# Optimization experiments

Hardware: AMD Instinct MI355X
Metric: run time of the kernel (lower is better)

## Reference

```python
import jax, jax.numpy as jnp
import numpy as np

RCUT = 6.0       # rcut
RMIN = 0.5       # rcut_smth
NF, NLOC, NALL, NNEI = 4, 4096, 4096, 128
AXIS = 8         # axis_neuron
EPS = 1e-12


def setup_inputs() -> dict:
    key = jax.random.key(0)
    ks = jax.random.split(key, 8)
    coord = jax.random.normal(ks[0], (NF, NALL, 3), dtype=jnp.float32) * 2.0
    nlist = jax.random.randint(ks[1], (NF, NLOC, NNEI), 0, NALL, dtype=jnp.int32)
    davg = jnp.zeros((NNEI, 4), dtype=jnp.float32)
    dstd = jnp.ones((NNEI, 4), dtype=jnp.float32)
    w1 = jax.random.normal(ks[2], (1, 24), dtype=jnp.float32) * 0.5
    b1 = jax.random.normal(ks[3], (24,), dtype=jnp.float32) * 0.1
    w2 = jax.random.normal(ks[4], (24, 48), dtype=jnp.float32) * 0.2
    b2 = jax.random.normal(ks[5], (48,), dtype=jnp.float32) * 0.1
    w3 = jax.random.normal(ks[6], (48, 96), dtype=jnp.float32) * 0.15
    b3 = jax.random.normal(ks[7], (96,), dtype=jnp.float32) * 0.1
    return {"coord": coord, "davg": davg, "dstd": dstd,
            "w1": w1, "b1": b1, "w2": w2, "b2": b2, "w3": w3, "b3": b3,
            "nlist": nlist}


def _embed(x, w1, b1, w2, b2, w3, b3):
    # DeepMD embedding net: tanh layers, resnet skip via duplication when dim doubles
    h1 = jnp.tanh(x @ w1 + b1)                                   # [..., 24]
    h2 = jnp.tanh(h1 @ w2 + b2) + jnp.concatenate([h1, h1], -1)  # [..., 48]
    h3 = jnp.tanh(h2 @ w3 + b3) + jnp.concatenate([h2, h2], -1)  # [..., 96]
    return h3


def reference(coord, davg, dstd, w1, b1, w2, b2, w3, b3, nlist):
    # gather neighbor coordinates: [nf, nloc, nnei, 3]
    coord_nei = jax.vmap(lambda c, nl: c[nl])(coord, nlist)
    rij = coord_nei - coord[:, :NLOC, None, :]
    r = jnp.sqrt(jnp.sum(rij * rij, axis=-1) + EPS)              # [nf, nloc, nnei]
    # smooth switching function
    uu = (r - RMIN) / (RCUT - RMIN)
    sw_mid = uu * uu * uu * (-6.0 * uu * uu + 15.0 * uu - 10.0) + 1.0
    sw = jnp.where(r < RMIN, 1.0, jnp.where(r < RCUT, sw_mid, 0.0))
    s = sw / r                                                    # [nf, nloc, nnei]
    # environment matrix R: [s, s*x/r, s*y/r, s*z/r] -> [nf, nloc, nnei, 4]
    env = jnp.concatenate([s[..., None], s[..., None] * rij / r[..., None]], axis=-1)
    env = (env - davg) / dstd
    # per-pair embedding of the radial channel
    G = _embed(env[..., :1], w1, b1, w2, b2, w3, b3)              # [nf, nloc, nnei, 96]
    # axis contraction: T = R^T G / nnei -> [nf, nloc, 4, 96]
    T = jnp.einsum('flnd,flnm->fldm', env, G) / NNEI
    # descriptor D = T^T T[:, :axis] -> [nf, nloc, 96, 8]
    D = jnp.einsum('fldm,fldk->flmk', T, T[..., :AXIS])
    return D.reshape(NF, NLOC, 96 * AXIS)
```

## Files before the change

kernel.cpp:

```cpp
#include <hip/hip_runtime.h>
#include <hip/hip_bf16.h>
#include <cstdint>

#define NF_   4
#define NLOC_ 4096
#define NALL_ 4096
#define NNEI_ 128
#define RCUT_ 6.0f
#define RMIN_ 0.5f

typedef __attribute__((ext_vector_type(8))) short    bhalf8;
typedef __attribute__((ext_vector_type(4))) float    f32x4;
typedef __attribute__((ext_vector_type(4))) unsigned u32x4;

__device__ __forceinline__ float fast_tanh(float x) {
    float e = __expf(2.0f * x);
    return 1.0f - 2.0f * __builtin_amdgcn_rcpf(e + 1.0f);
}
__device__ __forceinline__ unsigned short bfb(float v) {
    return __builtin_bit_cast(unsigned short, __float2bfloat16(v));
}
__device__ __forceinline__ float bff(unsigned short b) {
    return __builtin_bit_cast(float, (unsigned)b << 16);
}
__device__ __forceinline__ unsigned pk(float a, float b) {
    return (unsigned)bfb(a) | ((unsigned)bfb(b) << 16);
}
__device__ __forceinline__ float bf16_lo(unsigned u) {
    return __builtin_bit_cast(float, u << 16);
}
__device__ __forceinline__ float bf16_hi(unsigned u) {
    return __builtin_bit_cast(float, u & 0xffff0000u);
}

__global__ void prepack_weights(const float* __restrict__ w2,
                                const float* __restrict__ w3,
                                unsigned* __restrict__ ws) {
    const int idx = threadIdx.x + blockIdx.x * 256;
    if (idx < 768) {
        const int u   = idx & 3;
        const int l   = (idx >> 2) & 63;
        const int mt  = idx >> 8;
        const int m16 = l & 15, kg = l >> 4;
        const int k0  = 8 * kg + 2 * u;
        const unsigned short s0 = (k0 < 24)     ? bfb(w2[k0 * 48 + 16 * mt + m16])       : (unsigned short)0;
        const unsigned short s1 = (k0 + 1 < 24) ? bfb(w2[(k0 + 1) * 48 + 16 * mt + m16]) : (unsigned short)0;
        ws[idx] = (unsigned)s0 | ((unsigned)s1 << 16);
    } else if (idx < 3840) {
        const int j   = idx - 768;
        const int u   = j & 3;
        const int l   = (j >> 2) & 63;
        const int nt  = (j >> 8) & 1;
        const int ks  = (j >> 9) & 1;
        const int sb  = j >> 10;
        const int m16 = l & 15, kg = l >> 4;
        const int k0  = 32 * ks + 8 * kg + 2 * u;
        const int col = 32 * sb + 16 * nt + m16;
        const unsigned short s0 = (k0 < 48)     ? bfb(w3[k0 * 96 + col])       : (unsigned short)0;
        const unsigned short s1 = (k0 + 1 < 48) ? bfb(w3[(k0 + 1) * 96 + col]) : (unsigned short)0;
        ws[idx] = (unsigned)s0 | ((unsigned)s1 << 16);
    }
}

__global__ __launch_bounds__(128, 4)
void descrpt_sea_kernel(
    const float* __restrict__ coord,
    const float* __restrict__ davg,
    const float* __restrict__ dstd,
    const float* __restrict__ w1, const float* __restrict__ b1,
    const float* __restrict__ w2, const float* __restrict__ b2,
    const float* __restrict__ w3, const float* __restrict__ b3,
    const int*   __restrict__ nlist,
    const unsigned* __restrict__ wsp,
    float* __restrict__ out)
{
    __shared__ __align__(16) unsigned smem[6016];
    float*    envs = (float*)smem;
    unsigned* h1L  = smem + 512;
    unsigned* GsT  = smem;
    float*    Th2L = (float*)(smem + 2304);
    unsigned* h2L  = smem + 2688;
    float*    TyL  = (float*)(smem + 2688);
    float*    Ts   = (float*)(smem + 3456);

    const int t = threadIdx.x;
    const int a = blockIdx.x;
    const int f = a >> 12;
    const int i = a & 4095;

    const float* cf = coord + (size_t)f * (NALL_ * 3);
    const float cix = cf[i * 3 + 0];
    const float ciy = cf[i * 3 + 1];
    const float ciz = cf[i * 3 + 2];
    const int nbr = nlist[(size_t)a * NNEI_ + t];
    float dx = cf[nbr * 3 + 0] - cix;
    float dy = cf[nbr * 3 + 1] - ciy;
    float dz = cf[nbr * 3 + 2] - ciz;
    float r2 = fmaf(dx, dx, fmaf(dy, dy, dz * dz)) + 1e-12f;
    float r  = __builtin_amdgcn_sqrtf(r2);
    float rinv = __builtin_amdgcn_rcpf(r);
    float uu = (r - RMIN_) * (1.0f / (RCUT_ - RMIN_));
    float u2 = uu * uu;
    float mid = (uu * u2) * fmaf(-6.0f, u2, fmaf(15.0f, uu, -10.0f)) + 1.0f;
    float sw  = (r < RMIN_) ? 1.0f : ((r < RCUT_) ? mid : 0.0f);
    float sv  = sw * rinv;
    float e0 = sv;
    float e1 = sv * dx * rinv;
    float e2 = sv * dy * rinv;
    float e3 = sv * dz * rinv;
    const float4 da  = reinterpret_cast<const float4*>(davg)[t];
    const float4 dsd = reinterpret_cast<const float4*>(dstd)[t];
    e0 = (e0 - da.x) * __builtin_amdgcn_rcpf(dsd.x);
    e1 = (e1 - da.y) * __builtin_amdgcn_rcpf(dsd.y);
    e2 = (e2 - da.z) * __builtin_amdgcn_rcpf(dsd.z);
    e3 = (e3 - da.w) * __builtin_amdgcn_rcpf(dsd.w);
    envs[t * 4 + 0] = e0;
    envs[t * 4 + 1] = e1;
    envs[t * 4 + 2] = e2;
    envs[t * 4 + 3] = e3;

    {
        const float x = e0;
        float h1[24];
#pragma unroll
        for (int j = 0; j < 24; ++j)
            h1[j] = fast_tanh(fmaf(x, w1[j], b1[j]));
#pragma unroll
        for (int j = 0; j < 12; ++j)
            h1L[t * 14 + j] = pk(h1[2 * j], h1[2 * j + 1]);
    }
    __syncthreads();

    const int l   = t & 63;
    const int w   = t >> 6;
    const int m16 = l & 15;
    const int kg  = l >> 4;

    {
        bhalf8 w2A[3];
#pragma unroll
        for (int mt = 0; mt < 3; ++mt)
            w2A[mt] = __builtin_bit_cast(bhalf8, *(const u32x4*)&wsp[(mt * 64 + l) * 4]);

        f32x4 acc2[3][4];
#pragma unroll
        for (int mt = 0; mt < 3; ++mt) {
            const float4 bi = *(const float4*)&b2[16 * mt + 4 * kg];
#pragma unroll
            for (int nt = 0; nt < 4; ++nt)
                acc2[mt][nt] = (f32x4){bi.x, bi.y, bi.z, bi.w};
        }
#pragma unroll
        for (int nt = 0; nt < 4; ++nt) {
            bhalf8 bv;
            if (kg < 3) {
                const int p = 64 * w + 16 * nt + m16;
                const uint2 u01 = *(const uint2*)&h1L[p * 14 + 4 * kg];
                const uint2 u23 = *(const uint2*)&h1L[p * 14 + 4 * kg + 2];
                bv = __builtin_bit_cast(bhalf8, (u32x4){u01.x, u01.y, u23.x, u23.y});
            } else {
#pragma unroll
                for (int e = 0; e < 8; ++e) bv[e] = 0;
            }
#pragma unroll
            for (int mt = 0; mt < 3; ++mt)
                acc2[mt][nt] = __builtin_amdgcn_mfma_f32_16x16x32_bf16(
                    w2A[mt], bv, acc2[mt][nt], 0, 0, 0);
        }
#pragma unroll
        for (int nt = 0; nt < 4; ++nt) {
            const int p = 64 * w + 16 * nt + m16;
#pragma unroll
            for (int mt = 0; mt < 3; ++mt) {
                const int cbase = 16 * mt + 4 * kg;
                const int sbase = (cbase % 24) >> 1;
                const uint2 sk = *(const uint2*)&h1L[p * 14 + sbase];
                const float v0 = fast_tanh(acc2[mt][nt][0]) + bf16_lo(sk.x);
                const float v1 = fast_tanh(acc2[mt][nt][1]) + bf16_hi(sk.x);
                const float v2 = fast_tanh(acc2[mt][nt][2]) + bf16_lo(sk.y);
                const float v3 = fast_tanh(acc2[mt][nt][3]) + bf16_hi(sk.y);
                uint2 val;
                val.x = pk(v0, v1);
                val.y = pk(v2, v3);
                *(uint2*)&h2L[p * 26 + 8 * mt + 2 * kg] = val;
            }
        }
    }
    __syncthreads();

    bhalf8 envA[2];
#pragma unroll
    for (int ks = 0; ks < 2; ++ks) {
        bhalf8 av;
#pragma unroll
        for (int e = 0; e < 8; ++e) {
            const int row = 64 * w + 32 * ks + 8 * kg + e;
            const float v = envs[row * 4 + (m16 & 3)];
            const unsigned short hb = bfb(v);
            const unsigned short lb = bfb(v - bff(hb));
            const unsigned short sel = (m16 < 4) ? hb : ((m16 < 8) ? lb : (unsigned short)0);
            av[e] = (short)sel;
        }
        envA[ks] = av;
    }

    bhalf8 h2A[4][2];
#pragma unroll
    for (int mt = 0; mt < 4; ++mt) {
        const int row = 64 * w + 16 * mt + m16;
        {
            const int wbase = row * 26 + 4 * kg;
            const uint2 u01 = *(const uint2*)&h2L[wbase];
            const uint2 u23 = *(const uint2*)&h2L[wbase + 2];
            h2A[mt][0] = __builtin_bit_cast(bhalf8, (u32x4){u01.x, u01.y, u23.x, u23.y});
        }
        if (kg < 2) {
            const int wbase = row * 26 + 16 + 4 * kg;
            const uint2 u01 = *(const uint2*)&h2L[wbase];
            const uint2 u23 = *(const uint2*)&h2L[wbase + 2];
            h2A[mt][1] = __builtin_bit_cast(bhalf8, (u32x4){u01.x, u01.y, u23.x, u23.y});
        } else {
            bhalf8 z;
#pragma unroll
            for (int e = 0; e < 8; ++e) z[e] = 0;
            h2A[mt][1] = z;
        }
    }

#pragma unroll
    for (int nt = 0; nt < 3; ++nt) {
        f32x4 acc = {0.f, 0.f, 0.f, 0.f};
#pragma unroll
        for (int ks = 0; ks < 2; ++ks) {
            bhalf8 bv;
#pragma unroll
            for (int e = 0; e < 8; ++e) {
                const int row = 64 * w + 32 * ks + 8 * kg + e;
                const int col = 16 * nt + m16;
                const unsigned u = h2L[row * 26 + (col >> 1)];
                const unsigned short bits = (col & 1) ? (unsigned short)(u >> 16)
                                                      : (unsigned short)(u & 0xffffu);
                bv[e] = (short)bits;
            }
            acc = __builtin_amdgcn_mfma_f32_16x16x32_bf16(envA[ks], bv, acc, 0, 0, 0);
        }
#pragma unroll
        for (int rgi = 0; rgi < 4; ++rgi) {
            const float v = acc[rgi] + __shfl_down(acc[rgi], 16);
            if (kg == 0) Th2L[(w * 4 + rgi) * 48 + 16 * nt + m16] = v;
        }
    }
    __syncthreads();

#pragma unroll 1
    for (int sb = 0; sb < 3; ++sb) {
        const int nbase = 32 * sb;
        f32x4 acc[4][2];
#pragma unroll
        for (int nt = 0; nt < 2; ++nt) {
            const float b3v = b3[nbase + 16 * nt + m16];
#pragma unroll
            for (int mt = 0; mt < 4; ++mt)
                acc[mt][nt] = (f32x4){b3v, b3v, b3v, b3v};
        }
#pragma unroll
        for (int ks = 0; ks < 2; ++ks) {
#pragma unroll
            for (int nt = 0; nt < 2; ++nt) {
                const bhalf8 wb = __builtin_bit_cast(bhalf8,
                    *(const u32x4*)&wsp[768 + ((((sb * 2 + ks) * 2 + nt) * 64 + l) * 4)]);
#pragma unroll
                for (int mt = 0; mt < 4; ++mt)
                    acc[mt][nt] = __builtin_amdgcn_mfma_f32_16x16x32_bf16(
                        h2A[mt][ks], wb, acc[mt][nt], 0, 0, 0);
            }
        }
#pragma unroll
        for (int mt = 0; mt < 4; ++mt) {
#pragma unroll
            for (int nt = 0; nt < 2; ++nt) {
                const int col  = 16 * nt + m16;
                const int row0 = 64 * w + 16 * mt + 4 * kg;
                const float g0 = fast_tanh(acc[mt][nt][0]);
                const float g1 = fast_tanh(acc[mt][nt][1]);
                const float g2 = fast_tanh(acc[mt][nt][2]);
                const float g3 = fast_tanh(acc[mt][nt][3]);
                GsT[col * 66 + (row0 >> 1)]     = pk(g0, g1);
                GsT[col * 66 + (row0 >> 1) + 1] = pk(g2, g3);
            }
        }
        __syncthreads();
#pragma unroll
        for (int nt = 0; nt < 2; ++nt) {
            f32x4 ty = {0.f, 0.f, 0.f, 0.f};
#pragma unroll
            for (int ks = 0; ks < 2; ++ks) {
                const int col = 16 * nt + m16;
                const int wb2 = col * 66 + 32 * w + 16 * ks + 4 * kg;
                const uint2 u01 = *(const uint2*)&GsT[wb2];
                const uint2 u23 = *(const uint2*)&GsT[wb2 + 2];
                const bhalf8 bg = __builtin_bit_cast(bhalf8, (u32x4){u01.x, u01.y, u23.x, u23.y});
                ty = __builtin_amdgcn_mfma_f32_16x16x32_bf16(envA[ks], bg, ty, 0, 0, 0);
            }
#pragma unroll
            for (int rgi = 0; rgi < 4; ++rgi) {
                const float v = ty[rgi] + __shfl_down(ty[rgi], 16);
                if (kg == 0) TyL[(w * 4 + rgi) * 96 + nbase + 16 * nt + m16] = v;
            }
        }
        __syncthreads();
    }

#pragma unroll
    for (int j = 0; j < 3; ++j) {
        const int idx = t + 128 * j;
        const int d   = idx / 96;
        const int n   = idx - 96 * d;
        const int c   = (n >= 48) ? (n - 48) : n;
        const float v = TyL[(0 * 4 + d) * 96 + n] + TyL[(1 * 4 + d) * 96 + n]
                      + Th2L[(0 * 4 + d) * 48 + c] + Th2L[(1 * 4 + d) * 48 + c];
        Ts[d * 96 + n] = v * (1.0f / NNEI_);
    }
    __syncthreads();

    float* outp = out + (size_t)a * 768;
#pragma unroll
    for (int qq = 0; qq < 6; ++qq) {
        const int idx = t + 128 * qq;
        const int m = idx >> 3;
        const int k = idx & 7;
        const float d0 = Ts[0 * 96 + m] * Ts[0 * 96 + k];
        const float d1 = Ts[1 * 96 + m] * Ts[1 * 96 + k];
        const float d2 = Ts[2 * 96 + m] * Ts[2 * 96 + k];
        const float d3 = Ts[3 * 96 + m] * Ts[3 * 96 + k];
        outp[idx] = (d0 + d1) + (d2 + d3);
    }
}

extern "C" void kernel_launch(void* const* d_in, const int* in_sizes, int n_in,
                              void* d_out, int out_size, void* d_ws, size_t ws_size,
                              hipStream_t stream) {
    const float* coord = (const float*)d_in[0];
    const float* davg  = (const float*)d_in[1];
    const float* dstd  = (const float*)d_in[2];
    const float* w1    = (const float*)d_in[3];
    const float* b1    = (const float*)d_in[4];
    const float* w2    = (const float*)d_in[5];
    const float* b2    = (const float*)d_in[6];
    const float* w3    = (const float*)d_in[7];
    const float* b3    = (const float*)d_in[8];
    const int*   nlist = (const int*)d_in[9];
    float* outp = (float*)d_out;
    unsigned* wsp = (unsigned*)d_ws;

    prepack_weights<<<dim3(15), dim3(256), 0, stream>>>(w2, w3, wsp);
    descrpt_sea_kernel<<<dim3(NF_ * NLOC_), dim3(128), 0, stream>>>(
        coord, davg, dstd, w1, b1, w2, b2, w3, b3, nlist, wsp, outp);
}
```

Baseline: 239.7 us.

## Alias h2 buffer over env/h1 LDS region to shrink shared memory footprint

Moves the env and h1 reads into registers before a barrier so the h2 buffer can overwrite the env/h1 region, and relocates the Ty/Ts/Th2 scratch areas. This cuts shared memory per block from about 24KB to about 15KB, which could allow more resident blocks per CU. The cost is extra registers held across the layer-2 MFMA (bv, sk, envA), which may raise register pressure under the launch bound of 128 threads and 4 blocks.

```diff
diff --git a/kernel.cpp b/kernel.cpp
--- a/kernel.cpp
+++ b/kernel.cpp
@@ -74,14 +74,14 @@
     const unsigned* __restrict__ wsp,
     float* __restrict__ out)
 {
-    __shared__ __align__(16) unsigned smem[6016];
+    __shared__ __align__(16) unsigned smem[3712];
     float*    envs = (float*)smem;
     unsigned* h1L  = smem + 512;
+    unsigned* h2L  = smem;
     unsigned* GsT  = smem;
-    float*    Th2L = (float*)(smem + 2304);
-    unsigned* h2L  = smem + 2688;
-    float*    TyL  = (float*)(smem + 2688);
-    float*    Ts   = (float*)(smem + 3456);
+    float*    TyL  = (float*)(smem + 2112);
+    float*    Ts   = (float*)(smem + 2880);
+    float*    Th2L = (float*)(smem + 3328);
 
     const int t = threadIdx.x;
     const int a = blockIdx.x;
@@ -136,58 +136,6 @@
     const int m16 = l & 15;
     const int kg  = l >> 4;
 
-    {
-        bhalf8 w2A[3];
-#pragma unroll
-        for (int mt = 0; mt < 3; ++mt)
-            w2A[mt] = __builtin_bit_cast(bhalf8, *(const u32x4*)&wsp[(mt * 64 + l) * 4]);
-
-        f32x4 acc2[3][4];
-#pragma unroll
-        for (int mt = 0; mt < 3; ++mt) {
-            const float4 bi = *(const float4*)&b2[16 * mt + 4 * kg];
-#pragma unroll
-            for (int nt = 0; nt < 4; ++nt)
-                acc2[mt][nt] = (f32x4){bi.x, bi.y, bi.z, bi.w};
-        }
-#pragma unroll
-        for (int nt = 0; nt < 4; ++nt) {
-            bhalf8 bv;
-            if (kg < 3) {
-                const int p = 64 * w + 16 * nt + m16;
-                const uint2 u01 = *(const uint2*)&h1L[p * 14 + 4 * kg];
-                const uint2 u23 = *(const uint2*)&h1L[p * 14 + 4 * kg + 2];
-                bv = __builtin_bit_cast(bhalf8, (u32x4){u01.x, u01.y, u23.x, u23.y});
-            } else {
-#pragma unroll
-                for (int e = 0; e < 8; ++e) bv[e] = 0;
-            }
-#pragma unroll
-            for (int mt = 0; mt < 3; ++mt)
-                acc2[mt][nt] = __builtin_amdgcn_mfma_f32_16x16x32_bf16(
-                    w2A[mt], bv, acc2[mt][nt], 0, 0, 0);
-        }
-#pragma unroll
-        for (int nt = 0; nt < 4; ++nt) {
-            const int p = 64 * w + 16 * nt + m16;
-#pragma unroll
-            for (int mt = 0; mt < 3; ++mt) {
-                const int cbase = 16 * mt + 4 * kg;
-                const int sbase = (cbase % 24) >> 1;
-                const uint2 sk = *(const uint2*)&h1L[p * 14 + sbase];
-                const float v0 = fast_tanh(acc2[mt][nt][0]) + bf16_lo(sk.x);
-                const float v1 = fast_tanh(acc2[mt][nt][1]) + bf16_hi(sk.x);
-                const float v2 = fast_tanh(acc2[mt][nt][2]) + bf16_lo(sk.y);
-                const float v3 = fast_tanh(acc2[mt][nt][3]) + bf16_hi(sk.y);
-                uint2 val;
-                val.x = pk(v0, v1);
-                val.y = pk(v2, v3);
-                *(uint2*)&h2L[p * 26 + 8 * mt + 2 * kg] = val;
-            }
-        }
-    }
-    __syncthreads();
-
     bhalf8 envA[2];
 #pragma unroll
     for (int ks = 0; ks < 2; ++ks) {
@@ -203,6 +151,65 @@
         }
         envA[ks] = av;
     }
+    bhalf8 bv[4];
+    uint2  sk[4][3];
+#pragma unroll
+    for (int nt = 0; nt < 4; ++nt) {
+        const int p = 64 * w + 16 * nt + m16;
+        if (kg < 3) {
+            const uint2 u01 = *(const uint2*)&h1L[p * 14 + 4 * kg];
+            const uint2 u23 = *(const uint2*)&h1L[p * 14 + 4 * kg + 2];
+            bv[nt] = __builtin_bit_cast(bhalf8, (u32x4){u01.x, u01.y, u23.x, u23.y});
+        } else {
+            bhalf8 z;
+#pragma unroll
+            for (int e = 0; e < 8; ++e) z[e] = 0;
+            bv[nt] = z;
+        }
+        sk[nt][0] = *(const uint2*)&h1L[p * 14 + 2 * kg];
+        sk[nt][1] = *(const uint2*)&h1L[p * 14 + ((kg < 2) ? (8 + 2 * kg) : (2 * kg - 4))];
+        sk[nt][2] = *(const uint2*)&h1L[p * 14 + 4 + 2 * kg];
+    }
+    __syncthreads();
+
+    {
+        bhalf8 w2A[3];
+#pragma unroll
+        for (int mt = 0; mt < 3; ++mt)
+            w2A[mt] = __builtin_bit_cast(bhalf8, *(const u32x4*)&wsp[(mt * 64 + l) * 4]);
+
+        f32x4 acc2[3][4];
+#pragma unroll
+        for (int mt = 0; mt < 3; ++mt) {
+            const float4 bi = *(const float4*)&b2[16 * mt + 4 * kg];
+#pragma unroll
+            for (int nt = 0; nt < 4; ++nt)
+                acc2[mt][nt] = (f32x4){bi.x, bi.y, bi.z, bi.w};
+        }
+#pragma unroll
+        for (int nt = 0; nt < 4; ++nt) {
+#pragma unroll
+            for (int mt = 0; mt < 3; ++mt)
+                acc2[mt][nt] = __builtin_amdgcn_mfma_f32_16x16x32_bf16(
+                    w2A[mt], bv[nt], acc2[mt][nt], 0, 0, 0);
+        }
+#pragma unroll
+        for (int nt = 0; nt < 4; ++nt) {
+            const int p = 64 * w + 16 * nt + m16;
+#pragma unroll
+            for (int mt = 0; mt < 3; ++mt) {
+                const float v0 = fast_tanh(acc2[mt][nt][0]) + bf16_lo(sk[nt][mt].x);
+                const float v1 = fast_tanh(acc2[mt][nt][1]) + bf16_hi(sk[nt][mt].x);
+                const float v2 = fast_tanh(acc2[mt][nt][2]) + bf16_lo(sk[nt][mt].y);
+                const float v3 = fast_tanh(acc2[mt][nt][3]) + bf16_hi(sk[nt][mt].y);
+                uint2 val;
+                val.x = pk(v0, v1);
+                val.y = pk(v2, v3);
+                *(uint2*)&h2L[p * 26 + 8 * mt + 2 * kg] = val;
+            }
+        }
+    }
+    __syncthreads();
 
     bhalf8 h2A[4][2];
 #pragma unroll
@@ -232,7 +239,7 @@
         f32x4 acc = {0.f, 0.f, 0.f, 0.f};
 #pragma unroll
         for (int ks = 0; ks < 2; ++ks) {
-            bhalf8 bv;
+            bhalf8 bvv;
 #pragma unroll
             for (int e = 0; e < 8; ++e) {
                 const int row = 64 * w + 32 * ks + 8 * kg + e;
@@ -240,9 +247,9 @@
                 const unsigned u = h2L[row * 26 + (col >> 1)];
                 const unsigned short bits = (col & 1) ? (unsigned short)(u >> 16)
                                                       : (unsigned short)(u & 0xffffu);
-                bv[e] = (short)bits;
-            }
-            acc = __builtin_amdgcn_mfma_f32_16x16x32_bf16(envA[ks], bv, acc, 0, 0, 0);
+                bvv[e] = (short)bits;
+            }
+            acc = __builtin_amdgcn_mfma_f32_16x16x32_bf16(envA[ks], bvv, acc, 0, 0, 0);
         }
 #pragma unroll
         for (int rgi = 0; rgi < 4; ++rgi) {
```

New measurement: 219.5 us. -8.4%, faster.
